# Performance work log

Hardware: AMD Instinct MI355X
Metric: run time of the kernel (lower is better)

The kernel has to match this reference:

```python
import jax, jax.numpy as jnp
import numpy as np

B = 8192
D = 1024
NUM_CLASSES = 128
EPS = 1e-8  # torch F.cosine_similarity default eps


def setup_inputs() -> dict:
    key = jax.random.key(0)
    k1, k2, k3 = jax.random.split(key, 3)
    label_tensor = jax.random.randint(k1, (B,), 0, NUM_CLASSES, dtype=jnp.int64 if jax.config.jax_enable_x64 else jnp.int32)
    feature_a = jax.random.normal(k2, (B, D), dtype=jnp.float32)
    feature_b = jax.random.normal(k3, (B, D), dtype=jnp.float32)
    return {"label_tensor": label_tensor, "feature_a": feature_a, "feature_b": feature_b}


def reference(label_tensor, feature_a, feature_b):
    # Pairwise cosine similarity: cos_score[i, k] = cos(a_i, b_k), shape [B, B]
    dots = feature_a @ feature_b.T  # [B, B]
    na = jnp.linalg.norm(feature_a, axis=1)  # [B]
    nb = jnp.linalg.norm(feature_b, axis=1)  # [B]
    cos_score = dots / jnp.maximum(na[:, None] * nb[None, :], EPS)
    # Row-softmax (torch softmax dim=1 on the [B, B] matrix)
    logp = jax.nn.log_softmax(cos_score, axis=1)
    # Label-equality mask: positives for row i are all j with same label
    mask = (label_tensor[:, None] == label_tensor[None, :]).astype(cos_score.dtype)  # [B, B]
    per_row = -(mask * logp).sum(axis=1) / mask.sum(axis=1)  # diagonal guarantees >=1 positive
    loss = per_row.mean()
    return loss, cos_score
```

## Files before the change

kernel.cpp:

```cpp
#include <hip/hip_runtime.h>
#include <hip/hip_bf16.h>

#define NB 8192
#define ND 1024

typedef __bf16 bf16x8 __attribute__((ext_vector_type(8)));
typedef float  f32x4  __attribute__((ext_vector_type(4)));

__device__ inline void gload_lds16(const void* g, void* l) {
    __builtin_amdgcn_global_load_lds(
        (const __attribute__((address_space(1))) unsigned int*)g,
        (__attribute__((address_space(3))) unsigned int*)l,
        16, 0, 0);
}

__device__ inline unsigned short f2bf(float x) {
    unsigned int u = __float_as_uint(x);
    return (unsigned short)((u + 0x7fffu + ((u >> 16) & 1u)) >> 16);
}

#define BARRIER() asm volatile("s_barrier" ::: "memory")
#define VMCNT4()  asm volatile("s_waitcnt vmcnt(4)" ::: "memory")
#define VMCNT0()  asm volatile("s_waitcnt vmcnt(0)" ::: "memory")

__global__ __launch_bounds__(256) void prep_kernel(
    const float* __restrict__ A, const float* __restrict__ Bm,
    unsigned short* __restrict__ wa, unsigned short* __restrict__ wb,
    float* __restrict__ na, float* __restrict__ nb)
{
    int b = blockIdx.x;
    int wid = threadIdx.x >> 6, lane = threadIdx.x & 63;
    const float* src; unsigned short* dst; float* nrm; int row;
    if (b < 2048) { src = A;  dst = wa; nrm = na; row = b * 4 + wid; }
    else          { src = Bm; dst = wb; nrm = nb; row = (b - 2048) * 4 + wid; }

    const float*    rp = src + (size_t)row * ND;
    unsigned short* wp = dst + (size_t)row * ND;

    float ss = 0.f;
#pragma unroll
    for (int t = 0; t < 4; ++t) {
        int c = lane * 4 + t * 256;
        float4 v = *reinterpret_cast<const float4*>(rp + c);
        ss += v.x * v.x + v.y * v.y + v.z * v.z + v.w * v.w;
        ushort4 u;
        u.x = f2bf(v.x); u.y = f2bf(v.y); u.z = f2bf(v.z); u.w = f2bf(v.w);
        *reinterpret_cast<ushort4*>(wp + c) = u;
    }
#pragma unroll
    for (int off = 32; off; off >>= 1) ss += __shfl_xor(ss, off);
    if (lane == 0) nrm[row] = sqrtf(ss);
}

__global__ __launch_bounds__(256) void hist_kernel(
    const int* __restrict__ labels, int* __restrict__ hist)
{
    __shared__ int h[128];
    int tid = threadIdx.x;
    if (tid < 128) h[tid] = 0;
    __syncthreads();
    for (int i = tid; i < NB; i += 256) atomicAdd(&h[labels[i]], 1);
    __syncthreads();
    if (tid < 128) hist[tid] = h[tid];
}

__global__ __launch_bounds__(256) void gemm_cos(
    const unsigned short* __restrict__ wa, const unsigned short* __restrict__ wb,
    const float* __restrict__ na, const float* __restrict__ nb,
    const int* __restrict__ labels,
    float* __restrict__ C, float* __restrict__ pe, float* __restrict__ pm)
{
    __shared__ unsigned short lds[24576];

    const int bid = blockIdx.x;
    const int tm  = (bid & 7) * 8 + ((bid >> 3) & 7);
    const int tn  = bid >> 6;

    const int tid  = threadIdx.x;
    const int lane = tid & 63;
    const int wid  = tid >> 6;
    const int wr   = wid >> 1, wc = wid & 1;
    const int l15  = lane & 15, lg = lane >> 4;

    const int m0 = tm * 128, n0 = tn * 128;

    const int srow = tid >> 2;
    const int sg   = (tid & 3) ^ ((tid >> 3) & 3);
    const unsigned short* pA0 = wa + (size_t)(m0 + srow) * ND + sg * 8;
    const unsigned short* pA1 = pA0 + 64 * ND;
    const unsigned short* pB0 = wb + (size_t)(n0 + srow) * ND + sg * 8;
    const unsigned short* pB1 = pB0 + 64 * ND;
    const int stW = wid * 512;

    const int kg  = (lg ^ ((lane >> 1) & 3)) * 8;
    const int rdA = wr * 2048 + l15 * 32 + kg;
    const int rdB = 4096 + wc * 2048 + l15 * 32 + kg;

    f32x4 acc[4][4];
#pragma unroll
    for (int i = 0; i < 4; ++i)
#pragma unroll
        for (int j = 0; j < 4; ++j) acc[i][j] = (f32x4){0.f, 0.f, 0.f, 0.f};

#define STAGE(t, BUF) do { \
    gload_lds16(pA0 + (t) * 32, &lds[(BUF) + stW]); \
    gload_lds16(pA1 + (t) * 32, &lds[(BUF) + 2048 + stW]); \
    gload_lds16(pB0 + (t) * 32, &lds[(BUF) + 4096 + stW]); \
    gload_lds16(pB1 + (t) * 32, &lds[(BUF) + 6144 + stW]); } while (0)

#define COMPUTE(BUF) do { \
    bf16x8 bq[4], af[4]; \
    _Pragma("unroll") \
    for (int n_ = 0; n_ < 4; ++n_) \
        bq[n_] = *reinterpret_cast<const bf16x8*>(&lds[(BUF) + rdB + n_ * 512]); \
    _Pragma("unroll") \
    for (int m_ = 0; m_ < 4; ++m_) \
        af[m_] = *reinterpret_cast<const bf16x8*>(&lds[(BUF) + rdA + m_ * 512]); \
    _Pragma("unroll") \
    for (int m_ = 0; m_ < 4; ++m_) \
        _Pragma("unroll") \
        for (int n_ = 0; n_ < 4; ++n_) \
            acc[m_][n_] = __builtin_amdgcn_mfma_f32_16x16x32_bf16( \
                af[m_], bq[n_], acc[m_][n_], 0, 0, 0); \
    } while (0)

    STAGE(0, 0);
    STAGE(1, 8192);
    VMCNT4();
    BARRIER();

#pragma unroll
    for (int t = 0; t < 32; ++t) {
        const int cb  = (t % 3) * 8192;
        const int nb2 = ((t + 2) % 3) * 8192;
        if (t < 30) STAGE(t + 2, nb2);
        COMPUTE(cb);
        if (t < 29)      VMCNT4();
        else if (t < 31) VMCNT0();
        BARRIER();
    }

#undef COMPUTE
#undef STAGE

    __syncthreads();
    float* pl = reinterpret_cast<float*>(lds);

    float nbv[4]; int labc[4];
#pragma unroll
    for (int n = 0; n < 4; ++n) {
        int c = n0 + wc * 64 + n * 16 + l15;
        nbv[n] = nb[c]; labc[n] = labels[c];
    }

#pragma unroll
    for (int m = 0; m < 4; ++m) {
#pragma unroll
        for (int jj = 0; jj < 4; ++jj) {
            int rl = wr * 64 + m * 16 + lg * 4 + jj;
            int r  = m0 + rl;
            float nav = na[r]; int labr = labels[r];
            float es = 0.f, ms = 0.f;
#pragma unroll
            for (int n = 0; n < 4; ++n) {
                int c = n0 + wc * 64 + n * 16 + l15;
                float v = acc[m][n][jj] / fmaxf(nav * nbv[n], 1e-8f);
                C[(size_t)r * NB + c] = v;
                es += __expf(v);
                ms += (labc[n] == labr) ? v : 0.f;
            }
#pragma unroll
            for (int off = 1; off < 16; off <<= 1) {
                es += __shfl_xor(es, off);
                ms += __shfl_xor(ms, off);
            }
            if (l15 == 0) {
                int o = rl * 4 + wc * 2;
                pl[o] = es; pl[o + 1] = ms;
            }
        }
    }
    __syncthreads();
    if (tid < 128) {
        float es = pl[tid * 4]     + pl[tid * 4 + 2];
        float ms = pl[tid * 4 + 1] + pl[tid * 4 + 3];
        pe[tn * NB + m0 + tid] = es;
        pm[tn * NB + m0 + tid] = ms;
    }
}

__global__ __launch_bounds__(256) void loss_final(
    const float* __restrict__ pe, const float* __restrict__ pm,
    const int* __restrict__ labels, const int* __restrict__ hist,
    float* __restrict__ per_row)
{
    int row = blockIdx.x * 256 + threadIdx.x;
    float es = 0.f, ms = 0.f;
#pragma unroll
    for (int t = 0; t < 64; ++t) {
        es += pe[t * NB + row];
        ms += pm[t * NB + row];
    }
    per_row[row] = logf(es) - ms / (float)hist[labels[row]];
}

__global__ __launch_bounds__(256) void finalize(
    const float* __restrict__ per_row, float* __restrict__ out)
{
    __shared__ float sm[256];
    float s = 0.f;
    for (int i = threadIdx.x; i < NB; i += 256) s += per_row[i];
    sm[threadIdx.x] = s;
    __syncthreads();
    for (int k = 128; k; k >>= 1) {
        if (threadIdx.x < k) sm[threadIdx.x] += sm[threadIdx.x + k];
        __syncthreads();
    }
    if (threadIdx.x == 0) out[0] = sm[0] * (1.0f / (float)NB);
}

extern "C" void kernel_launch(void* const* d_in, const int* in_sizes, int n_in,
                              void* d_out, int out_size, void* d_ws, size_t ws_size,
                              hipStream_t stream) {
    const int*   labels = (const int*)d_in[0];
    const float* A      = (const float*)d_in[1];
    const float* Bm     = (const float*)d_in[2];
    float* out = (float*)d_out;

    char* ws = (char*)d_ws;
    unsigned short* wa = (unsigned short*)(ws);
    unsigned short* wb = (unsigned short*)(ws + 16777216);
    float* na      = (float*)(ws + 33554432);
    float* nb      = (float*)(ws + 33554432 + 32768);
    float* per_row = (float*)(ws + 33554432 + 65536);
    int*   hist    = (int*)  (ws + 33554432 + 98304);
    float* pe      = (float*)(ws + 33554432 + 131072);
    float* pm      = (float*)(ws + 33554432 + 131072 + 2097152);

    float* cosm = out + 1;

    prep_kernel<<<4096, 256, 0, stream>>>(A, Bm, wa, wb, na, nb);
    hist_kernel<<<1,    256, 0, stream>>>(labels, hist);
    gemm_cos   <<<4096, 256, 0, stream>>>(wa, wb, na, nb, labels, cosm, pe, pm);
    loss_final <<<32,   256, 0, stream>>>(pe, pm, labels, hist, per_row);
    finalize   <<<1,    256, 0, stream>>>(per_row, out);
}
```

Before: 271.7 us.

## Enlarge GEMM tile to 256x128 with 8x4 MFMA accumulators per wave

```diff
diff --git a/kernel.cpp b/kernel.cpp
--- a/kernel.cpp
+++ b/kernel.cpp
@@ -20,8 +20,9 @@
 }
 
 #define BARRIER() asm volatile("s_barrier" ::: "memory")
-#define VMCNT4()  asm volatile("s_waitcnt vmcnt(4)" ::: "memory")
+#define VMCNT6()  asm volatile("s_waitcnt vmcnt(6)" ::: "memory")
 #define VMCNT0()  asm volatile("s_waitcnt vmcnt(0)" ::: "memory")
+#define LGKM0()   asm volatile("s_waitcnt lgkmcnt(0)" ::: "memory")
 
 __global__ __launch_bounds__(256) void prep_kernel(
     const float* __restrict__ A, const float* __restrict__ Bm,
@@ -64,49 +65,51 @@
     if (tid < 128) hist[tid] = h[tid];
 }
 
-__global__ __launch_bounds__(256) void gemm_cos(
+__global__ __launch_bounds__(256, 2) void gemm_cos(
     const unsigned short* __restrict__ wa, const unsigned short* __restrict__ wb,
     const float* __restrict__ na, const float* __restrict__ nb,
     const int* __restrict__ labels,
     float* __restrict__ C, float* __restrict__ pe, float* __restrict__ pm)
 {
-    __shared__ unsigned short lds[24576];
+    __shared__ unsigned short lds[36864];
 
     const int bid = blockIdx.x;
-    const int tm  = (bid & 7) * 8 + ((bid >> 3) & 7);
-    const int tn  = bid >> 6;
+    const int tm  = (bid & 7) * 4 + ((bid >> 3) & 3);
+    const int tn  = bid >> 5;
 
     const int tid  = threadIdx.x;
     const int lane = tid & 63;
     const int wid  = tid >> 6;
-    const int wr   = wid >> 1, wc = wid & 1;
+    const int wr   = wid & 1, wc = wid >> 1;
     const int l15  = lane & 15, lg = lane >> 4;
 
-    const int m0 = tm * 128, n0 = tn * 128;
+    const int m0 = tm * 256, n0 = tn * 128;
 
     const int srow = tid >> 2;
     const int sg   = (tid & 3) ^ ((tid >> 3) & 3);
-    const unsigned short* pA0 = wa + (size_t)(m0 + srow) * ND + sg * 8;
-    const unsigned short* pA1 = pA0 + 64 * ND;
-    const unsigned short* pB0 = wb + (size_t)(n0 + srow) * ND + sg * 8;
-    const unsigned short* pB1 = pB0 + 64 * ND;
+    const unsigned short* pA = wa + (size_t)(m0 + srow) * ND + sg * 8;
+    const unsigned short* pB = wb + (size_t)(n0 + srow) * ND + sg * 8;
     const int stW = wid * 512;
 
     const int kg  = (lg ^ ((lane >> 1) & 3)) * 8;
-    const int rdA = wr * 2048 + l15 * 32 + kg;
-    const int rdB = 4096 + wc * 2048 + l15 * 32 + kg;
-
-    f32x4 acc[4][4];
-#pragma unroll
-    for (int i = 0; i < 4; ++i)
+    const int rdA = wr * 4096 + l15 * 32 + kg;
+    const int rdB = 8192 + (wc * 64 + l15) * 32 + kg;
+
+    f32x4 acc[8][4];
+#pragma unroll
+    for (int i = 0; i < 8; ++i)
 #pragma unroll
         for (int j = 0; j < 4; ++j) acc[i][j] = (f32x4){0.f, 0.f, 0.f, 0.f};
 
 #define STAGE(t, BUF) do { \
-    gload_lds16(pA0 + (t) * 32, &lds[(BUF) + stW]); \
-    gload_lds16(pA1 + (t) * 32, &lds[(BUF) + 2048 + stW]); \
-    gload_lds16(pB0 + (t) * 32, &lds[(BUF) + 4096 + stW]); \
-    gload_lds16(pB1 + (t) * 32, &lds[(BUF) + 6144 + stW]); } while (0)
+    _Pragma("unroll") \
+    for (int c_ = 0; c_ < 4; ++c_) \
+        gload_lds16(pA + (size_t)c_ * 64 * ND + (t) * 32, \
+                    &lds[(BUF) + c_ * 2048 + stW]); \
+    _Pragma("unroll") \
+    for (int c_ = 0; c_ < 2; ++c_) \
+        gload_lds16(pB + (size_t)c_ * 64 * ND + (t) * 32, \
+                    &lds[(BUF) + 8192 + c_ * 2048 + stW]); } while (0)
 
 #define COMPUTE(BUF) do { \
     bf16x8 bq[4], af[4]; \
@@ -122,21 +125,31 @@
         for (int n_ = 0; n_ < 4; ++n_) \
             acc[m_][n_] = __builtin_amdgcn_mfma_f32_16x16x32_bf16( \
                 af[m_], bq[n_], acc[m_][n_], 0, 0, 0); \
+    _Pragma("unroll") \
+    for (int m_ = 0; m_ < 4; ++m_) \
+        af[m_] = *reinterpret_cast<const bf16x8*>(&lds[(BUF) + rdA + 2048 + m_ * 512]); \
+    _Pragma("unroll") \
+    for (int m_ = 0; m_ < 4; ++m_) \
+        _Pragma("unroll") \
+        for (int n_ = 0; n_ < 4; ++n_) \
+            acc[4 + m_][n_] = __builtin_amdgcn_mfma_f32_16x16x32_bf16( \
+                af[m_], bq[n_], acc[4 + m_][n_], 0, 0, 0); \
     } while (0)
 
     STAGE(0, 0);
-    STAGE(1, 8192);
-    VMCNT4();
+    STAGE(1, 12288);
+    VMCNT6();
     BARRIER();
 
 #pragma unroll
     for (int t = 0; t < 32; ++t) {
-        const int cb  = (t % 3) * 8192;
-        const int nb2 = ((t + 2) % 3) * 8192;
+        const int cb  = (t % 3) * 12288;
+        const int nb2 = ((t + 2) % 3) * 12288;
         if (t < 30) STAGE(t + 2, nb2);
         COMPUTE(cb);
-        if (t < 29)      VMCNT4();
+        if (t < 30)      VMCNT6();
         else if (t < 31) VMCNT0();
+        LGKM0();
         BARRIER();
     }
 
@@ -154,10 +167,10 @@
     }
 
 #pragma unroll
-    for (int m = 0; m < 4; ++m) {
+    for (int m = 0; m < 8; ++m) {
 #pragma unroll
         for (int jj = 0; jj < 4; ++jj) {
-            int rl = wr * 64 + m * 16 + lg * 4 + jj;
+            int rl = wr * 128 + m * 16 + lg * 4 + jj;
             int r  = m0 + rl;
             float nav = na[r]; int labr = labels[r];
             float es = 0.f, ms = 0.f;
@@ -181,7 +194,7 @@
         }
     }
     __syncthreads();
-    if (tid < 128) {
+    if (tid < 256) {
         float es = pl[tid * 4]     + pl[tid * 4 + 2];
         float ms = pl[tid * 4 + 1] + pl[tid * 4 + 3];
         pe[tn * NB + m0 + tid] = es;
@@ -241,7 +254,7 @@
 
     prep_kernel<<<4096, 256, 0, stream>>>(A, Bm, wa, wb, na, nb);
     hist_kernel<<<1,    256, 0, stream>>>(labels, hist);
-    gemm_cos   <<<4096, 256, 0, stream>>>(wa, wb, na, nb, labels, cosm, pe, pm);
+    gemm_cos   <<<2048, 256, 0, stream>>>(wa, wb, na, nb, labels, cosm, pe, pm);
     loss_final <<<32,   256, 0, stream>>>(pe, pm, labels, hist, per_row);
     finalize   <<<1,    256, 0, stream>>>(per_row, out);
 }
```

New measurement: 270.3 us. No clear change (-0.5%).
